# Optimization experiments

Measured on AMD Instinct MI355X. Metric: run time of the kernel, lower is better.

Reference implementation:

```python
import itertools
import jax, jax.numpy as jnp
import numpy as np

# ---- constant tables / bases ----
Y_TABLE_NP = np.array([
    [16, 11, 10, 16, 24, 40, 51, 61],
    [12, 12, 14, 19, 26, 58, 60, 55],
    [14, 13, 16, 24, 40, 57, 69, 56],
    [14, 17, 22, 29, 51, 87, 80, 62],
    [18, 22, 37, 56, 68, 109, 103, 77],
    [24, 35, 55, 64, 81, 104, 113, 92],
    [49, 64, 78, 87, 103, 121, 120, 101],
    [72, 92, 95, 98, 112, 100, 103, 99]], dtype=np.float32)
C_TABLE_NP = np.full((8, 8), 99, dtype=np.float32)
C_TABLE_NP[:4, :4] = np.array([[17, 18, 24, 47], [18, 21, 26, 66],
                               [24, 26, 56, 99], [47, 66, 99, 99]], dtype=np.float32)

def _bases():
    dct = np.zeros((8, 8, 8, 8), dtype=np.float32)
    idct = np.zeros((8, 8, 8, 8), dtype=np.float32)
    for x, y, u, v in itertools.product(range(8), repeat=4):
        dct[x, y, u, v] = np.cos((2 * x + 1) * u * np.pi / 16) * np.cos((2 * y + 1) * v * np.pi / 16)
        idct[x, y, u, v] = np.cos((2 * u + 1) * x * np.pi / 16) * np.cos((2 * v + 1) * y * np.pi / 16)
    alpha = np.array([1.0 / np.sqrt(2)] + [1.0] * 7, dtype=np.float32)
    ao = np.outer(alpha, alpha).astype(np.float32)
    return jnp.asarray(dct), jnp.asarray(ao * 0.25), jnp.asarray(idct), jnp.asarray(ao)

DCT_T, DCT_SCALE, IDCT_T, ALPHA = _bases()
FACTOR = 0.4  # quality_to_factor(80) = (200 - 2*80)/100


def diff_round(x):
    r = jnp.round(x)
    return r + (x - r) ** 3


def _blocks(img):  # (B,H,W) -> (B, H*W/64, 8, 8)
    B, H, W = img.shape
    return img.reshape(B, H // 8, 8, W // 8, 8).transpose(0, 1, 3, 2, 4).reshape(B, -1, 8, 8)


def _merge(patches, H, W):  # (B, N, 8, 8) -> (B, H, W)
    B = patches.shape[0]
    return patches.reshape(B, H // 8, W // 8, 8, 8).transpose(0, 1, 3, 2, 4).reshape(B, H, W)


def setup_inputs() -> dict:
    key = jax.random.key(0)
    image = jax.random.uniform(key, (32, 3, 512, 512), dtype=jnp.float32)
    return {"image": image,
            "y_table": jnp.asarray(Y_TABLE_NP),
            "c_table": jnp.asarray(C_TABLE_NP)}


def reference(image, y_table, c_table):
    B, _, H, W = image.shape
    x = image * 255.0
    # RGB -> YCbCr (matrix stored transposed in torch, tensordot over channel)
    rgb2ycc = jnp.array([[0.299, 0.587, 0.114],
                         [-0.168736, -0.331264, 0.5],
                         [0.5, -0.418688, -0.081312]], dtype=jnp.float32)
    shift = jnp.array([0.0, 128.0, 128.0], dtype=jnp.float32)
    ycc = jnp.einsum('bchw,kc->bhwk', x, rgb2ycc) + shift  # (B,H,W,3)
    y = ycc[..., 0]
    # chroma subsampling: 2x2 average pool
    def pool2(ch):
        return ch.reshape(B, H // 2, 2, W // 2, 2).mean(axis=(2, 4))
    cb = pool2(ycc[..., 1])
    cr = pool2(ycc[..., 2])

    def compress(ch, table):
        blk = _blocks(ch) - 128.0
        d = DCT_SCALE * jnp.einsum('bnxy,xyuv->bnuv', blk, DCT_T)
        return diff_round(d / (table * FACTOR))

    yq = compress(y, y_table)
    cbq = compress(cb, c_table)
    crq = compress(cr, c_table)

    def decompress(q, table, h, w):
        d = (q * (table * FACTOR)) * ALPHA
        blk = 0.25 * jnp.einsum('bnuv,uvxy->bnxy', d, IDCT_T) + 128.0
        return _merge(blk, h, w)

    y_rec = decompress(yq, y_table, H, W)
    cb_rec = decompress(cbq, c_table, H // 2, W // 2)
    cr_rec = decompress(crq, c_table, H // 2, W // 2)

    def up2(ch):
        b, h, w = ch.shape
        return jnp.broadcast_to(ch[:, :, None, :, None], (b, h, 2, w, 2)).reshape(b, 2 * h, 2 * w)

    ycc_rec = jnp.stack([y_rec, up2(cb_rec), up2(cr_rec)], axis=-1)  # (B,H,W,3)
    ycc2rgb = jnp.array([[1.0, 0.0, 1.402],
                         [1.0, -0.344136, -0.714136],
                         [1.0, 1.772, 0.0]], dtype=jnp.float32)
    shift2 = jnp.array([0.0, -128.0, -128.0], dtype=jnp.float32)
    rgb = jnp.einsum('bhwk,ck->bhwc', ycc_rec + shift2, ycc2rgb)
    rgb = rgb.transpose(0, 3, 1, 2)  # (B,3,H,W)
    return jnp.clip(rgb, 0.0, 255.0) / 255.0
```

## Files before the change

kernel.cpp:

```cpp
#include <hip/hip_runtime.h>
#include <math.h>

#define IMG_H 512
#define IMG_W 512
#define IMG_HW (IMG_H * IMG_W)

namespace {

constexpr float CFv[9] = {
    1.0f,
    0.98078528040323044913f,
    0.92387953251128675613f,
    0.83146961230254523708f,
    0.70710678118654752440f,
    0.55557023301960222474f,
    0.38268343236508977173f,
    0.19509032201612826785f,
    0.0f
};

struct CTab {
    float  cf[8][8];
    double cd[8][8];
    float  aof[8][8];
    float  scalef[8][8];
};

constexpr CTab make_ctab() {
    CTab t{};
    for (int y = 0; y < 8; y++) {
        for (int v = 0; v < 8; v++) {
            int a = ((2 * y + 1) * v) & 31;
            if (a > 16) a = 32 - a;
            float val = (a <= 8) ? CFv[a] : -CFv[16 - a];
            t.cf[y][v] = val;
            t.cd[y][v] = (double)val;
        }
    }
    constexpr float A0 = 0.70710678118654752440f;
    for (int u = 0; u < 8; u++) {
        for (int v = 0; v < 8; v++) {
            float au = (u == 0) ? A0 : 1.0f;
            float av = (v == 0) ? A0 : 1.0f;
            float ao = au * av;
            t.aof[u][v] = ao;
            t.scalef[u][v] = ao * 0.25f;
        }
    }
    return t;
}

constexpr CTab CT = make_ctab();

__device__ __forceinline__ void fwd8_d(const double a[8], double s[8]) {
    double e0 = a[0] + a[7], e1 = a[1] + a[6], e2 = a[2] + a[5], e3 = a[3] + a[4];
    double o0 = a[0] - a[7], o1 = a[1] - a[6], o2 = a[2] - a[5], o3 = a[3] - a[4];
    double ee0 = e0 + e3, ee1 = e1 + e2, eo0 = e0 - e3, eo1 = e1 - e2;
    s[0] = ee0 + ee1;
    s[4] = (ee0 - ee1) * CT.cd[0][4];
    s[2] = eo0 * CT.cd[0][2] + eo1 * CT.cd[1][2];
    s[6] = eo0 * CT.cd[0][6] + eo1 * CT.cd[1][6];
    #pragma unroll
    for (int k = 0; k < 4; k++) {
        const int v = 2 * k + 1;
        s[v] = o0 * CT.cd[0][v] + o1 * CT.cd[1][v] + o2 * CT.cd[2][v] + o3 * CT.cd[3][v];
    }
}

__device__ __forceinline__ void inv8_f(const float d[8], float m[8]) {
    float eea = fmaf(CT.cf[0][4], d[4], d[0]);
    float eeb = fmaf(CT.cf[1][4], d[4], d[0]);
    float u2a = d[2] * CT.cf[0][2] + d[6] * CT.cf[0][6];
    float u2b = d[2] * CT.cf[1][2] + d[6] * CT.cf[1][6];
    float E0 = eea + u2a, E1 = eeb + u2b, E2 = eeb - u2b, E3 = eea - u2a;
    float O0 = d[1] * CT.cf[0][1] + d[3] * CT.cf[0][3] + d[5] * CT.cf[0][5] + d[7] * CT.cf[0][7];
    float O1 = d[1] * CT.cf[1][1] + d[3] * CT.cf[1][3] + d[5] * CT.cf[1][5] + d[7] * CT.cf[1][7];
    float O2 = d[1] * CT.cf[2][1] + d[3] * CT.cf[2][3] + d[5] * CT.cf[2][5] + d[7] * CT.cf[2][7];
    float O3 = d[1] * CT.cf[3][1] + d[3] * CT.cf[3][3] + d[5] * CT.cf[3][5] + d[7] * CT.cf[3][7];
    m[0] = E0 + O0; m[7] = E0 - O0;
    m[1] = E1 + O1; m[6] = E1 - O1;
    m[2] = E2 + O2; m[5] = E2 - O2;
    m[3] = E3 + O3; m[4] = E3 - O3;
}

}

#define OFF_CBP 8448
#define OFF_CRP 10624
#define OFF_QYF 12800
#define OFF_QCF 13440
#define OFF_DSY 14080
#define OFF_DSC 14464
#define OFF_CBR 4352
#define OFF_CRR 5504
#define SMEM_BYTES 14848

__global__ void __launch_bounds__(256, 6) djpeg_kernel(
    const float* __restrict__ img,
    const float* __restrict__ ytab,
    const float* __restrict__ ctab,
    float* __restrict__ out)
{
    __shared__ __align__(16) unsigned char smem[SMEM_BYTES];
    double* lY   = (double*)(smem);
    double* cbP  = (double*)(smem + OFF_CBP);
    double* crP  = (double*)(smem + OFF_CRP);
    double* qYfs = (double*)(smem + OFF_QYF);
    double* qCfs = (double*)(smem + OFF_QCF);
    float*  dsY  = (float*)(smem + OFF_DSY);
    float*  dsC  = (float*)(smem + OFF_DSC);
    float*  yR   = (float*)(smem);
    float*  cbR  = (float*)(smem + OFF_CBR);
    float*  crR  = (float*)(smem + OFF_CRR);

    const int t  = threadIdx.x;
    const int X0 = blockIdx.x * 64;
    const int Y0 = blockIdx.y * 16;
    const int bi = blockIdx.z;

    if (t < 128) {
        const float* tab = (t < 64) ? ytab : ctab;
        double* qf = (t < 64) ? qYfs : qCfs;
        float*  df = (t < 64) ? dsY : dsC;
        int e = t & 63, u = e >> 3, v = e & 7;
        float tfacf = tab[e] * 0.4f;
        double tf = (double)tfacf;
        qf[v * 10 + u] = (double)CT.scalef[u][v] / tf;
        df[v * 12 + u] = (float)(tf * (double)CT.aof[u][v]);
    }

    {
        const int xq = t & 15, yb = t >> 4;
        size_t base = ((size_t)bi * 3) * IMG_HW + (size_t)(Y0 + yb) * IMG_W + X0 + xq * 4;
        const float4 rf = *(const float4*)(img + base);
        const float4 gf = *(const float4*)(img + base + IMG_HW);
        const float4 bf = *(const float4*)(img + base + 2 * IMG_HW);
        const double kYR =  (double)0.299f    * 255.0, kYG =  (double)0.587f    * 255.0, kYB =  (double)0.114f    * 255.0;
        const double kbR = -(double)0.168736f * 255.0, kbG = -(double)0.331264f * 255.0, kbB =  (double)0.5f      * 255.0;
        const double krR =  (double)0.5f      * 255.0, krG = -(double)0.418688f * 255.0, krB = -(double)0.081312f * 255.0;
        const float rr[4] = {rf.x, rf.y, rf.z, rf.w};
        const float gg[4] = {gf.x, gf.y, gf.z, gf.w};
        const float bb[4] = {bf.x, bf.y, bf.z, bf.w};
        double Yv[4], Cbv[4], Crv[4];
        #pragma unroll
        for (int i = 0; i < 4; i++) {
            double R = (double)rr[i], G = (double)gg[i], B = (double)bb[i];
            Yv[i]  = kYR * R + kYG * G + kYB * B;
            Cbv[i] = kbR * R + kbG * G + kbB * B + 128.0;
            Crv[i] = krR * R + krG * G + krB * B + 128.0;
        }
        double2* yw = (double2*)(lY + yb * 66 + xq * 4);
        yw[0] = make_double2(Yv[0], Yv[1]);
        yw[1] = make_double2(Yv[2], Yv[3]);
        double cb0 = Cbv[0] + Cbv[1], cb1 = Cbv[2] + Cbv[3];
        double cr0 = Crv[0] + Crv[1], cr1 = Crv[2] + Crv[3];
        cb0 += __shfl_xor(cb0, 16);
        cb1 += __shfl_xor(cb1, 16);
        cr0 += __shfl_xor(cr0, 16);
        cr1 += __shfl_xor(cr1, 16);
        if ((yb & 1) == 0) {
            int pr = yb >> 1;
            *(double2*)(cbP + pr * 34 + xq * 2) = make_double2(cb0 * 0.25, cb1 * 0.25);
            *(double2*)(crP + pr * 34 + xq * 2) = make_double2(cr0 * 0.25, cr1 * 0.25);
        }
    }
    __syncthreads();

    const bool act = (t < 192);
    const int r = t & 7;
    double* blkd = lY;  const double* qfp = qYfs;  const float* dfp = dsY;
    float*  blkf = yR;
    int sD = 66, sF = 68;
    if (t < 128) {
        int g = t >> 3, by = g >> 3, bx = g & 7;
        blkd = lY + (by * 8) * 66 + bx * 8;
        blkf = yR + (by * 8) * 68 + bx * 8;
    } else if (t < 192) {
        int c = t - 128, isCr = c >> 5, g2 = (c >> 3) & 3;
        blkd = (isCr ? crP : cbP) + g2 * 8;
        blkf = (isCr ? crR : cbR) + g2 * 8;
        qfp = qCfs; dfp = dsC;
        sD = 34; sF = 36;
    }

    float dq[8];
    if (act) {
        const double* sp = blkd + r * sD;
        const double2 a01 = *(const double2*)(sp + 0);
        const double2 a23 = *(const double2*)(sp + 2);
        const double2 a45 = *(const double2*)(sp + 4);
        const double2 a67 = *(const double2*)(sp + 6);
        const double a[8] = {a01.x, a01.y, a23.x, a23.y, a45.x, a45.y, a67.x, a67.y};
        double s1[8];
        fwd8_d(a, s1);
        s1[0] -= 1024.0;

        #pragma unroll
        for (int v = 0; v < 8; v++) blkd[v * sD + r] = s1[v];
        asm volatile("s_waitcnt lgkmcnt(0)" ::: "memory");
        const double* rp = blkd + r * sD;
        const double2 b01 = *(const double2*)(rp + 0);
        const double2 b23 = *(const double2*)(rp + 2);
        const double2 b45 = *(const double2*)(rp + 4);
        const double2 b67 = *(const double2*)(rp + 6);
        const double s2[8] = {b01.x, b01.y, b23.x, b23.y, b45.x, b45.y, b67.x, b67.y};

        double D[8];
        fwd8_d(s2, D);
        const double2 f01 = *(const double2*)(qfp + r * 10 + 0);
        const double2 f23 = *(const double2*)(qfp + r * 10 + 2);
        const double2 f45 = *(const double2*)(qfp + r * 10 + 4);
        const double2 f67 = *(const double2*)(qfp + r * 10 + 6);
        const double fsv[8] = {f01.x, f01.y, f23.x, f23.y, f45.x, f45.y, f67.x, f67.y};
        const float4 dA = *(const float4*)(dfp + r * 12);
        const float4 dB = *(const float4*)(dfp + r * 12 + 4);
        const float dsv[8] = {dA.x, dA.y, dA.z, dA.w, dB.x, dB.y, dB.z, dB.w};
        #pragma unroll
        for (int u = 0; u < 8; u++) {
            double xq = D[u] * fsv[u];
            double rq = rint(xq);
            float ef  = (float)(xq - rq);
            float rqf = (float)rq;
            dq[u] = (rqf + ef * ef * ef) * dsv[u];
        }
    }

    __syncthreads();

    if (act) {
        float mc[8];
        inv8_f(dq, mc);

        #pragma unroll
        for (int p = 0; p < 8; p++) blkf[p * sF + r] = mc[p];
        asm volatile("s_waitcnt lgkmcnt(0)" ::: "memory");
        const float* fp_ = blkf + r * sF;
        const float4 m0 = *(const float4*)(fp_);
        const float4 m1 = *(const float4*)(fp_ + 4);
        const float mrow[8] = {m0.x, m0.y, m0.z, m0.w, m1.x, m1.y, m1.z, m1.w};

        float px[8];
        inv8_f(mrow, px);
        float* fw = blkf + r * sF;
        *(float4*)(fw)     = make_float4(fmaf(0.25f, px[0], 128.0f), fmaf(0.25f, px[1], 128.0f),
                                         fmaf(0.25f, px[2], 128.0f), fmaf(0.25f, px[3], 128.0f));
        *(float4*)(fw + 4) = make_float4(fmaf(0.25f, px[4], 128.0f), fmaf(0.25f, px[5], 128.0f),
                                         fmaf(0.25f, px[6], 128.0f), fmaf(0.25f, px[7], 128.0f));
    }
    __syncthreads();

    {
        const int xq = t & 15, yb = t >> 4;
        const float4 yv  = *(const float4*)(yR + yb * 68 + xq * 4);
        const float2 cbv = *(const float2*)(cbR + (yb >> 1) * 36 + xq * 2);
        const float2 crv = *(const float2*)(crR + (yb >> 1) * 36 + xq * 2);
        const float yy[4]  = {yv.x, yv.y, yv.z, yv.w};
        const float cbs[2] = {cbv.x - 128.0f, cbv.y - 128.0f};
        const float crs[2] = {crv.x - 128.0f, crv.y - 128.0f};
        float R4[4], G4[4], B4[4];
        #pragma unroll
        for (int i = 0; i < 4; i++) {
            float Yv = yy[i], Cb = cbs[i >> 1], Cr = crs[i >> 1];
            float Rr = Yv + 1.402f * Cr;
            float Gg = Yv - 0.344136f * Cb - 0.714136f * Cr;
            float Bb = Yv + 1.772f * Cb;
            R4[i] = fminf(fmaxf(Rr, 0.0f), 255.0f) * (1.0f / 255.0f);
            G4[i] = fminf(fmaxf(Gg, 0.0f), 255.0f) * (1.0f / 255.0f);
            B4[i] = fminf(fmaxf(Bb, 0.0f), 255.0f) * (1.0f / 255.0f);
        }
        size_t base = ((size_t)bi * 3) * IMG_HW + (size_t)(Y0 + yb) * IMG_W + X0 + xq * 4;
        *(float4*)(out + base)              = make_float4(R4[0], R4[1], R4[2], R4[3]);
        *(float4*)(out + base + IMG_HW)     = make_float4(G4[0], G4[1], G4[2], G4[3]);
        *(float4*)(out + base + 2 * IMG_HW) = make_float4(B4[0], B4[1], B4[2], B4[3]);
    }
}

extern "C" void kernel_launch(void* const* d_in, const int* in_sizes, int n_in,
                              void* d_out, int out_size, void* d_ws, size_t ws_size,
                              hipStream_t stream) {
    (void)n_in; (void)out_size; (void)d_ws; (void)ws_size;
    const float* img = (const float*)d_in[0];
    const float* yt  = (const float*)d_in[1];
    const float* ct  = (const float*)d_in[2];
    float* out = (float*)d_out;
    int B = in_sizes[0] / (3 * IMG_HW);
    dim3 grid(IMG_W / 64, IMG_H / 16, B);
    djpeg_kernel<<<grid, dim3(256, 1, 1), 0, stream>>>(img, yt, ct, out);
}
```

Baseline: 181.6 us.

## Partition block into per-wave 16x16 tiles and drop block-wide barriers

Each 64-lane wave now owns its own 16x16 pixel tile in shared memory and handles four Y blocks plus one Cb and one Cr block. This removes two of the three block-wide barriers between phases, replacing them with lgkmcnt waits, and the global image loads are hoisted above the table setup so they overlap it. Launch bounds rise from 6 to 8 blocks per CU and shared memory grows slightly. The cost is that 16 of 64 lanes per wave sit idle during the DCT phases, and global loads now cover 16-float row segments instead of 64.

```diff
diff --git a/kernel.cpp b/kernel.cpp
--- a/kernel.cpp
+++ b/kernel.cpp
@@ -85,38 +85,47 @@
 
 }
 
-#define OFF_CBP 8448
-#define OFF_CRP 10624
-#define OFF_QYF 12800
-#define OFF_QCF 13440
-#define OFF_DSY 14080
-#define OFF_DSC 14464
-#define OFF_CBR 4352
-#define OFF_CRR 5504
-#define SMEM_BYTES 14848
-
-__global__ void __launch_bounds__(256, 6) djpeg_kernel(
+#define WAVE_BYTES 3584
+#define OFF_CBP 2304
+#define OFF_CRP 2944
+#define OFF_CBR 1280
+#define OFF_CRR 1664
+#define OFF_QYF 14336
+#define OFF_QCF 14976
+#define OFF_DSY 15616
+#define OFF_DSC 16000
+#define SMEM_BYTES 16384
+
+__global__ void __launch_bounds__(256, 8) djpeg_kernel(
     const float* __restrict__ img,
     const float* __restrict__ ytab,
     const float* __restrict__ ctab,
     float* __restrict__ out)
 {
     __shared__ __align__(16) unsigned char smem[SMEM_BYTES];
-    double* lY   = (double*)(smem);
-    double* cbP  = (double*)(smem + OFF_CBP);
-    double* crP  = (double*)(smem + OFF_CRP);
+    const int t = threadIdx.x;
+    const int w = t >> 6, l = t & 63;
+    unsigned char* wb = smem + w * WAVE_BYTES;
+    double* lYd = (double*)wb;
+    double* cbP = (double*)(wb + OFF_CBP);
+    double* crP = (double*)(wb + OFF_CRP);
+    float*  yR  = (float*)wb;
+    float*  cbR = (float*)(wb + OFF_CBR);
+    float*  crR = (float*)(wb + OFF_CRR);
     double* qYfs = (double*)(smem + OFF_QYF);
     double* qCfs = (double*)(smem + OFF_QCF);
     float*  dsY  = (float*)(smem + OFF_DSY);
     float*  dsC  = (float*)(smem + OFF_DSC);
-    float*  yR   = (float*)(smem);
-    float*  cbR  = (float*)(smem + OFF_CBR);
-    float*  crR  = (float*)(smem + OFF_CRR);
-
-    const int t  = threadIdx.x;
-    const int X0 = blockIdx.x * 64;
+
+    const int bi = blockIdx.z;
+    const int X0 = blockIdx.x * 64 + w * 16;
     const int Y0 = blockIdx.y * 16;
-    const int bi = blockIdx.z;
+    const int q = l & 3, row = l >> 2;
+
+    const size_t base = ((size_t)bi * 3) * IMG_HW + (size_t)(Y0 + row) * IMG_W + X0 + q * 4;
+    const float4 rf = *(const float4*)(img + base);
+    const float4 gf = *(const float4*)(img + base + IMG_HW);
+    const float4 bf = *(const float4*)(img + base + 2 * IMG_HW);
 
     if (t < 128) {
         const float* tab = (t < 64) ? ytab : ctab;
@@ -128,63 +137,56 @@
         qf[v * 10 + u] = (double)CT.scalef[u][v] / tf;
         df[v * 12 + u] = (float)(tf * (double)CT.aof[u][v]);
     }
+    __syncthreads();
 
     {
-        const int xq = t & 15, yb = t >> 4;
-        size_t base = ((size_t)bi * 3) * IMG_HW + (size_t)(Y0 + yb) * IMG_W + X0 + xq * 4;
-        const float4 rf = *(const float4*)(img + base);
-        const float4 gf = *(const float4*)(img + base + IMG_HW);
-        const float4 bf = *(const float4*)(img + base + 2 * IMG_HW);
         const double kYR =  (double)0.299f    * 255.0, kYG =  (double)0.587f    * 255.0, kYB =  (double)0.114f    * 255.0;
         const double kbR = -(double)0.168736f * 255.0, kbG = -(double)0.331264f * 255.0, kbB =  (double)0.5f      * 255.0;
         const double krR =  (double)0.5f      * 255.0, krG = -(double)0.418688f * 255.0, krB = -(double)0.081312f * 255.0;
         const float rr[4] = {rf.x, rf.y, rf.z, rf.w};
         const float gg[4] = {gf.x, gf.y, gf.z, gf.w};
         const float bb[4] = {bf.x, bf.y, bf.z, bf.w};
-        double Yv[4], Cbv[4], Crv[4];
+        double Yv[4];
+        double cb0 = 0.0, cb1 = 0.0, cr0 = 0.0, cr1 = 0.0;
         #pragma unroll
         for (int i = 0; i < 4; i++) {
             double R = (double)rr[i], G = (double)gg[i], B = (double)bb[i];
-            Yv[i]  = kYR * R + kYG * G + kYB * B;
-            Cbv[i] = kbR * R + kbG * G + kbB * B + 128.0;
-            Crv[i] = krR * R + krG * G + krB * B + 128.0;
-        }
-        double2* yw = (double2*)(lY + yb * 66 + xq * 4);
+            Yv[i] = kYR * R + kYG * G + kYB * B;
+            double Cb = kbR * R + kbG * G + kbB * B + 128.0;
+            double Cr = krR * R + krG * G + krB * B + 128.0;
+            if (i < 2) { cb0 += Cb; cr0 += Cr; } else { cb1 += Cb; cr1 += Cr; }
+        }
+        double2* yw = (double2*)(lYd + row * 18 + q * 4);
         yw[0] = make_double2(Yv[0], Yv[1]);
         yw[1] = make_double2(Yv[2], Yv[3]);
-        double cb0 = Cbv[0] + Cbv[1], cb1 = Cbv[2] + Cbv[3];
-        double cr0 = Crv[0] + Crv[1], cr1 = Crv[2] + Crv[3];
-        cb0 += __shfl_xor(cb0, 16);
-        cb1 += __shfl_xor(cb1, 16);
-        cr0 += __shfl_xor(cr0, 16);
-        cr1 += __shfl_xor(cr1, 16);
-        if ((yb & 1) == 0) {
-            int pr = yb >> 1;
-            *(double2*)(cbP + pr * 34 + xq * 2) = make_double2(cb0 * 0.25, cb1 * 0.25);
-            *(double2*)(crP + pr * 34 + xq * 2) = make_double2(cr0 * 0.25, cr1 * 0.25);
-        }
-    }
-    __syncthreads();
-
-    const bool act = (t < 192);
-    const int r = t & 7;
-    double* blkd = lY;  const double* qfp = qYfs;  const float* dfp = dsY;
-    float*  blkf = yR;
-    int sD = 66, sF = 68;
-    if (t < 128) {
-        int g = t >> 3, by = g >> 3, bx = g & 7;
-        blkd = lY + (by * 8) * 66 + bx * 8;
-        blkf = yR + (by * 8) * 68 + bx * 8;
-    } else if (t < 192) {
-        int c = t - 128, isCr = c >> 5, g2 = (c >> 3) & 3;
-        blkd = (isCr ? crP : cbP) + g2 * 8;
-        blkf = (isCr ? crR : cbR) + g2 * 8;
+        cb0 += __shfl_xor(cb0, 4);
+        cb1 += __shfl_xor(cb1, 4);
+        cr0 += __shfl_xor(cr0, 4);
+        cr1 += __shfl_xor(cr1, 4);
+        if ((row & 1) == 0) {
+            const int pr = row >> 1;
+            *(double2*)(cbP + pr * 10 + q * 2) = make_double2(cb0 * 0.25, cb1 * 0.25);
+            *(double2*)(crP + pr * 10 + q * 2) = make_double2(cr0 * 0.25, cr1 * 0.25);
+        }
+    }
+    asm volatile("s_waitcnt lgkmcnt(0)" ::: "memory");
+
+    const int g = l >> 3, r = l & 7;
+    double* blkd = lYd;  float* blkf = yR;
+    const double* qfp = qYfs;  const float* dfp = dsY;
+    int sD = 18, sF = 20;
+    if (g < 4) {
+        const int by = g >> 1, bx = g & 1;
+        blkd = lYd + by * 144 + bx * 8;
+        blkf = yR  + by * 160 + bx * 8;
+    } else {
+        blkd = (g == 5) ? crP : cbP;
+        blkf = (g == 5) ? crR : cbR;
         qfp = qCfs; dfp = dsC;
-        sD = 34; sF = 36;
-    }
-
-    float dq[8];
-    if (act) {
+        sD = 10; sF = 12;
+    }
+
+    if (g < 6) {
         const double* sp = blkd + r * sD;
         const double2 a01 = *(const double2*)(sp + 0);
         const double2 a23 = *(const double2*)(sp + 2);
@@ -215,6 +217,7 @@
         const float4 dA = *(const float4*)(dfp + r * 12);
         const float4 dB = *(const float4*)(dfp + r * 12 + 4);
         const float dsv[8] = {dA.x, dA.y, dA.z, dA.w, dB.x, dB.y, dB.z, dB.w};
+        float dq[8];
         #pragma unroll
         for (int u = 0; u < 8; u++) {
             double xq = D[u] * fsv[u];
@@ -223,11 +226,7 @@
             float rqf = (float)rq;
             dq[u] = (rqf + ef * ef * ef) * dsv[u];
         }
-    }
-
-    __syncthreads();
-
-    if (act) {
+
         float mc[8];
         inv8_f(dq, mc);
 
@@ -247,13 +246,12 @@
         *(float4*)(fw + 4) = make_float4(fmaf(0.25f, px[4], 128.0f), fmaf(0.25f, px[5], 128.0f),
                                          fmaf(0.25f, px[6], 128.0f), fmaf(0.25f, px[7], 128.0f));
     }
-    __syncthreads();
+    asm volatile("s_waitcnt lgkmcnt(0)" ::: "memory");
 
     {
-        const int xq = t & 15, yb = t >> 4;
-        const float4 yv  = *(const float4*)(yR + yb * 68 + xq * 4);
-        const float2 cbv = *(const float2*)(cbR + (yb >> 1) * 36 + xq * 2);
-        const float2 crv = *(const float2*)(crR + (yb >> 1) * 36 + xq * 2);
+        const float4 yv  = *(const float4*)(yR + row * 20 + q * 4);
+        const float2 cbv = *(const float2*)(cbR + (row >> 1) * 12 + q * 2);
+        const float2 crv = *(const float2*)(crR + (row >> 1) * 12 + q * 2);
         const float yy[4]  = {yv.x, yv.y, yv.z, yv.w};
         const float cbs[2] = {cbv.x - 128.0f, cbv.y - 128.0f};
         const float crs[2] = {crv.x - 128.0f, crv.y - 128.0f};
@@ -268,7 +266,6 @@
             G4[i] = fminf(fmaxf(Gg, 0.0f), 255.0f) * (1.0f / 255.0f);
             B4[i] = fminf(fmaxf(Bb, 0.0f), 255.0f) * (1.0f / 255.0f);
         }
-        size_t base = ((size_t)bi * 3) * IMG_HW + (size_t)(Y0 + yb) * IMG_W + X0 + xq * 4;
         *(float4*)(out + base)              = make_float4(R4[0], R4[1], R4[2], R4[3]);
         *(float4*)(out + base + IMG_HW)     = make_float4(G4[0], G4[1], G4[2], G4[3]);
         *(float4*)(out + base + 2 * IMG_HW) = make_float4(B4[0], B4[1], B4[2], B4[3]);
```

After: 185.7 us. +2.3%, slower.

## Process two 16-row strips per block to amortize setup and overlap loads

Applied to the files above, without the earlier changes.

Each block now handles a 64x32 tile as two 16-row strips with separate shared-memory buffers, halving the grid. All six global float4 loads are issued up front, before the quantization-table setup, so their latency overlaps that setup. The table setup, barriers and launch overhead are amortized over twice the work, and per-thread ILP rises from interleaving two independent DCT pipelines. In exchange shared memory nearly doubles, register pressure rises, and launch bounds drop from 6 to 5 blocks per CU, which may lower occupancy.

```diff
diff --git a/kernel.cpp b/kernel.cpp
--- a/kernel.cpp
+++ b/kernel.cpp
@@ -85,38 +85,55 @@
 
 }
 
+#define STRIP_BYTES 12800
 #define OFF_CBP 8448
 #define OFF_CRP 10624
-#define OFF_QYF 12800
-#define OFF_QCF 13440
-#define OFF_DSY 14080
-#define OFF_DSC 14464
 #define OFF_CBR 4352
 #define OFF_CRR 5504
-#define SMEM_BYTES 14848
-
-__global__ void __launch_bounds__(256, 6) djpeg_kernel(
+#define OFF_QYF 25600
+#define OFF_QCF 26240
+#define OFF_DSY 26880
+#define OFF_DSC 27264
+#define SMEM_BYTES 27648
+
+__global__ void __launch_bounds__(256, 5) djpeg_kernel(
     const float* __restrict__ img,
     const float* __restrict__ ytab,
     const float* __restrict__ ctab,
     float* __restrict__ out)
 {
     __shared__ __align__(16) unsigned char smem[SMEM_BYTES];
-    double* lY   = (double*)(smem);
-    double* cbP  = (double*)(smem + OFF_CBP);
-    double* crP  = (double*)(smem + OFF_CRP);
+    double* lY0  = (double*)(smem);
+    double* cbP0 = (double*)(smem + OFF_CBP);
+    double* crP0 = (double*)(smem + OFF_CRP);
+    float*  yR0  = (float*)(smem);
+    float*  cbR0 = (float*)(smem + OFF_CBR);
+    float*  crR0 = (float*)(smem + OFF_CRR);
+    double* lY1  = (double*)(smem + STRIP_BYTES);
+    double* cbP1 = (double*)(smem + STRIP_BYTES + OFF_CBP);
+    double* crP1 = (double*)(smem + STRIP_BYTES + OFF_CRP);
+    float*  yR1  = (float*)(smem + STRIP_BYTES);
+    float*  cbR1 = (float*)(smem + STRIP_BYTES + OFF_CBR);
+    float*  crR1 = (float*)(smem + STRIP_BYTES + OFF_CRR);
     double* qYfs = (double*)(smem + OFF_QYF);
     double* qCfs = (double*)(smem + OFF_QCF);
     float*  dsY  = (float*)(smem + OFF_DSY);
     float*  dsC  = (float*)(smem + OFF_DSC);
-    float*  yR   = (float*)(smem);
-    float*  cbR  = (float*)(smem + OFF_CBR);
-    float*  crR  = (float*)(smem + OFF_CRR);
 
     const int t  = threadIdx.x;
     const int X0 = blockIdx.x * 64;
-    const int Y0 = blockIdx.y * 16;
+    const int Y0 = blockIdx.y * 32;
     const int bi = blockIdx.z;
+    const int xq = t & 15, yb = t >> 4;
+
+    const size_t base0 = ((size_t)bi * 3) * IMG_HW + (size_t)(Y0 + yb) * IMG_W + X0 + xq * 4;
+    const size_t base1 = base0 + (size_t)16 * IMG_W;
+    const float4 rf0 = *(const float4*)(img + base0);
+    const float4 gf0 = *(const float4*)(img + base0 + IMG_HW);
+    const float4 bf0 = *(const float4*)(img + base0 + 2 * IMG_HW);
+    const float4 rf1 = *(const float4*)(img + base1);
+    const float4 gf1 = *(const float4*)(img + base1 + IMG_HW);
+    const float4 bf1 = *(const float4*)(img + base1 + 2 * IMG_HW);
 
     if (t < 128) {
         const float* tab = (t < 64) ? ytab : ctab;
@@ -129,128 +146,179 @@
         df[v * 12 + u] = (float)(tf * (double)CT.aof[u][v]);
     }
 
-    {
-        const int xq = t & 15, yb = t >> 4;
-        size_t base = ((size_t)bi * 3) * IMG_HW + (size_t)(Y0 + yb) * IMG_W + X0 + xq * 4;
-        const float4 rf = *(const float4*)(img + base);
-        const float4 gf = *(const float4*)(img + base + IMG_HW);
-        const float4 bf = *(const float4*)(img + base + 2 * IMG_HW);
+    auto phase1 = [&](const float4 rf, const float4 gf, const float4 bf,
+                      double* lY, double* cbP, double* crP) {
         const double kYR =  (double)0.299f    * 255.0, kYG =  (double)0.587f    * 255.0, kYB =  (double)0.114f    * 255.0;
         const double kbR = -(double)0.168736f * 255.0, kbG = -(double)0.331264f * 255.0, kbB =  (double)0.5f      * 255.0;
         const double krR =  (double)0.5f      * 255.0, krG = -(double)0.418688f * 255.0, krB = -(double)0.081312f * 255.0;
         const float rr[4] = {rf.x, rf.y, rf.z, rf.w};
         const float gg[4] = {gf.x, gf.y, gf.z, gf.w};
         const float bb[4] = {bf.x, bf.y, bf.z, bf.w};
-        double Yv[4], Cbv[4], Crv[4];
+        double Yv[4];
+        double cb0 = 0.0, cb1 = 0.0, cr0 = 0.0, cr1 = 0.0;
         #pragma unroll
         for (int i = 0; i < 4; i++) {
             double R = (double)rr[i], G = (double)gg[i], B = (double)bb[i];
-            Yv[i]  = kYR * R + kYG * G + kYB * B;
-            Cbv[i] = kbR * R + kbG * G + kbB * B + 128.0;
-            Crv[i] = krR * R + krG * G + krB * B + 128.0;
+            Yv[i] = kYR * R + kYG * G + kYB * B;
+            double Cb = kbR * R + kbG * G + kbB * B + 128.0;
+            double Cr = krR * R + krG * G + krB * B + 128.0;
+            if (i < 2) { cb0 += Cb; cr0 += Cr; } else { cb1 += Cb; cr1 += Cr; }
         }
         double2* yw = (double2*)(lY + yb * 66 + xq * 4);
         yw[0] = make_double2(Yv[0], Yv[1]);
         yw[1] = make_double2(Yv[2], Yv[3]);
-        double cb0 = Cbv[0] + Cbv[1], cb1 = Cbv[2] + Cbv[3];
-        double cr0 = Crv[0] + Crv[1], cr1 = Crv[2] + Crv[3];
         cb0 += __shfl_xor(cb0, 16);
         cb1 += __shfl_xor(cb1, 16);
         cr0 += __shfl_xor(cr0, 16);
         cr1 += __shfl_xor(cr1, 16);
         if ((yb & 1) == 0) {
-            int pr = yb >> 1;
+            const int pr = yb >> 1;
             *(double2*)(cbP + pr * 34 + xq * 2) = make_double2(cb0 * 0.25, cb1 * 0.25);
             *(double2*)(crP + pr * 34 + xq * 2) = make_double2(cr0 * 0.25, cr1 * 0.25);
         }
-    }
+    };
+    phase1(rf0, gf0, bf0, lY0, cbP0, crP0);
+    phase1(rf1, gf1, bf1, lY1, cbP1, crP1);
     __syncthreads();
 
     const bool act = (t < 192);
     const int r = t & 7;
-    double* blkd = lY;  const double* qfp = qYfs;  const float* dfp = dsY;
-    float*  blkf = yR;
-    int sD = 66, sF = 68;
+    int eD = 0, eF = 0, sD = 66, sF = 68;
+    const double* qfp = qYfs;  const float* dfp = dsY;
     if (t < 128) {
         int g = t >> 3, by = g >> 3, bx = g & 7;
-        blkd = lY + (by * 8) * 66 + bx * 8;
-        blkf = yR + (by * 8) * 68 + bx * 8;
-    } else if (t < 192) {
+        eD = (by * 8) * 66 + bx * 8;
+        eF = (by * 8) * 68 + bx * 8;
+    } else {
         int c = t - 128, isCr = c >> 5, g2 = (c >> 3) & 3;
-        blkd = (isCr ? crP : cbP) + g2 * 8;
-        blkf = (isCr ? crR : cbR) + g2 * 8;
+        eD = (isCr ? (OFF_CRP / 8) : (OFF_CBP / 8)) + g2 * 8;
+        eF = (isCr ? (OFF_CRR / 4) : (OFF_CBR / 4)) + g2 * 8;
         qfp = qCfs; dfp = dsC;
         sD = 34; sF = 36;
     }
-
-    float dq[8];
+    double* bdA = lY0 + eD;  double* bdB = lY1 + eD;
+    float*  bfA = yR0 + eF;  float*  bfB = yR1 + eF;
+
+    float dqA[8], dqB[8];
     if (act) {
-        const double* sp = blkd + r * sD;
-        const double2 a01 = *(const double2*)(sp + 0);
-        const double2 a23 = *(const double2*)(sp + 2);
-        const double2 a45 = *(const double2*)(sp + 4);
-        const double2 a67 = *(const double2*)(sp + 6);
-        const double a[8] = {a01.x, a01.y, a23.x, a23.y, a45.x, a45.y, a67.x, a67.y};
-        double s1[8];
-        fwd8_d(a, s1);
-        s1[0] -= 1024.0;
-
-        #pragma unroll
-        for (int v = 0; v < 8; v++) blkd[v * sD + r] = s1[v];
+        {
+            const double* sp = bdA + r * sD;
+            const double2 a01 = *(const double2*)(sp + 0);
+            const double2 a23 = *(const double2*)(sp + 2);
+            const double2 a45 = *(const double2*)(sp + 4);
+            const double2 a67 = *(const double2*)(sp + 6);
+            const double a[8] = {a01.x, a01.y, a23.x, a23.y, a45.x, a45.y, a67.x, a67.y};
+            double s1[8];
+            fwd8_d(a, s1);
+            s1[0] -= 1024.0;
+            #pragma unroll
+            for (int v = 0; v < 8; v++) bdA[v * sD + r] = s1[v];
+        }
+        {
+            const double* sp = bdB + r * sD;
+            const double2 a01 = *(const double2*)(sp + 0);
+            const double2 a23 = *(const double2*)(sp + 2);
+            const double2 a45 = *(const double2*)(sp + 4);
+            const double2 a67 = *(const double2*)(sp + 6);
+            const double a[8] = {a01.x, a01.y, a23.x, a23.y, a45.x, a45.y, a67.x, a67.y};
+            double s1[8];
+            fwd8_d(a, s1);
+            s1[0] -= 1024.0;
+            #pragma unroll
+            for (int v = 0; v < 8; v++) bdB[v * sD + r] = s1[v];
+        }
         asm volatile("s_waitcnt lgkmcnt(0)" ::: "memory");
-        const double* rp = blkd + r * sD;
-        const double2 b01 = *(const double2*)(rp + 0);
-        const double2 b23 = *(const double2*)(rp + 2);
-        const double2 b45 = *(const double2*)(rp + 4);
-        const double2 b67 = *(const double2*)(rp + 6);
-        const double s2[8] = {b01.x, b01.y, b23.x, b23.y, b45.x, b45.y, b67.x, b67.y};
-
-        double D[8];
-        fwd8_d(s2, D);
+
         const double2 f01 = *(const double2*)(qfp + r * 10 + 0);
         const double2 f23 = *(const double2*)(qfp + r * 10 + 2);
         const double2 f45 = *(const double2*)(qfp + r * 10 + 4);
         const double2 f67 = *(const double2*)(qfp + r * 10 + 6);
         const double fsv[8] = {f01.x, f01.y, f23.x, f23.y, f45.x, f45.y, f67.x, f67.y};
-        const float4 dA = *(const float4*)(dfp + r * 12);
-        const float4 dB = *(const float4*)(dfp + r * 12 + 4);
-        const float dsv[8] = {dA.x, dA.y, dA.z, dA.w, dB.x, dB.y, dB.z, dB.w};
+        const float4 dA4 = *(const float4*)(dfp + r * 12);
+        const float4 dB4 = *(const float4*)(dfp + r * 12 + 4);
+        const float dsv[8] = {dA4.x, dA4.y, dA4.z, dA4.w, dB4.x, dB4.y, dB4.z, dB4.w};
+
+        {
+            const double* rp = bdA + r * sD;
+            const double2 b01 = *(const double2*)(rp + 0);
+            const double2 b23 = *(const double2*)(rp + 2);
+            const double2 b45 = *(const double2*)(rp + 4);
+            const double2 b67 = *(const double2*)(rp + 6);
+            const double s2[8] = {b01.x, b01.y, b23.x, b23.y, b45.x, b45.y, b67.x, b67.y};
+            double D[8];
+            fwd8_d(s2, D);
+            #pragma unroll
+            for (int u = 0; u < 8; u++) {
+                double xqv = D[u] * fsv[u];
+                double rq = rint(xqv);
+                float ef  = (float)(xqv - rq);
+                float rqf = (float)rq;
+                dqA[u] = (rqf + ef * ef * ef) * dsv[u];
+            }
+        }
+        {
+            const double* rp = bdB + r * sD;
+            const double2 b01 = *(const double2*)(rp + 0);
+            const double2 b23 = *(const double2*)(rp + 2);
+            const double2 b45 = *(const double2*)(rp + 4);
+            const double2 b67 = *(const double2*)(rp + 6);
+            const double s2[8] = {b01.x, b01.y, b23.x, b23.y, b45.x, b45.y, b67.x, b67.y};
+            double D[8];
+            fwd8_d(s2, D);
+            #pragma unroll
+            for (int u = 0; u < 8; u++) {
+                double xqv = D[u] * fsv[u];
+                double rq = rint(xqv);
+                float ef  = (float)(xqv - rq);
+                float rqf = (float)rq;
+                dqB[u] = (rqf + ef * ef * ef) * dsv[u];
+            }
+        }
+    }
+
+    __syncthreads();
+
+    if (act) {
+        float mcA[8], mcB[8];
+        inv8_f(dqA, mcA);
+        inv8_f(dqB, mcB);
         #pragma unroll
-        for (int u = 0; u < 8; u++) {
-            double xq = D[u] * fsv[u];
-            double rq = rint(xq);
-            float ef  = (float)(xq - rq);
-            float rqf = (float)rq;
-            dq[u] = (rqf + ef * ef * ef) * dsv[u];
-        }
-    }
-
+        for (int p = 0; p < 8; p++) bfA[p * sF + r] = mcA[p];
+        #pragma unroll
+        for (int p = 0; p < 8; p++) bfB[p * sF + r] = mcB[p];
+        asm volatile("s_waitcnt lgkmcnt(0)" ::: "memory");
+
+        {
+            const float* fp_ = bfA + r * sF;
+            const float4 m0 = *(const float4*)(fp_);
+            const float4 m1 = *(const float4*)(fp_ + 4);
+            const float mrow[8] = {m0.x, m0.y, m0.z, m0.w, m1.x, m1.y, m1.z, m1.w};
+            float px[8];
+            inv8_f(mrow, px);
+            float* fw = bfA + r * sF;
+            *(float4*)(fw)     = make_float4(fmaf(0.25f, px[0], 128.0f), fmaf(0.25f, px[1], 128.0f),
+                                             fmaf(0.25f, px[2], 128.0f), fmaf(0.25f, px[3], 128.0f));
+            *(float4*)(fw + 4) = make_float4(fmaf(0.25f, px[4], 128.0f), fmaf(0.25f, px[5], 128.0f),
+                                             fmaf(0.25f, px[6], 128.0f), fmaf(0.25f, px[7], 128.0f));
+        }
+        {
+            const float* fp_ = bfB + r * sF;
+            const float4 m0 = *(const float4*)(fp_);
+            const float4 m1 = *(const float4*)(fp_ + 4);
+            const float mrow[8] = {m0.x, m0.y, m0.z, m0.w, m1.x, m1.y, m1.z, m1.w};
+            float px[8];
+            inv8_f(mrow, px);
+            float* fw = bfB + r * sF;
+            *(float4*)(fw)     = make_float4(fmaf(0.25f, px[0], 128.0f), fmaf(0.25f, px[1], 128.0f),
+                                             fmaf(0.25f, px[2], 128.0f), fmaf(0.25f, px[3], 128.0f));
+            *(float4*)(fw + 4) = make_float4(fmaf(0.25f, px[4], 128.0f), fmaf(0.25f, px[5], 128.0f),
+                                             fmaf(0.25f, px[6], 128.0f), fmaf(0.25f, px[7], 128.0f));
+        }
+    }
     __syncthreads();
 
-    if (act) {
-        float mc[8];
-        inv8_f(dq, mc);
-
-        #pragma unroll
-        for (int p = 0; p < 8; p++) blkf[p * sF + r] = mc[p];
-        asm volatile("s_waitcnt lgkmcnt(0)" ::: "memory");
-        const float* fp_ = blkf + r * sF;
-        const float4 m0 = *(const float4*)(fp_);
-        const float4 m1 = *(const float4*)(fp_ + 4);
-        const float mrow[8] = {m0.x, m0.y, m0.z, m0.w, m1.x, m1.y, m1.z, m1.w};
-
-        float px[8];
-        inv8_f(mrow, px);
-        float* fw = blkf + r * sF;
-        *(float4*)(fw)     = make_float4(fmaf(0.25f, px[0], 128.0f), fmaf(0.25f, px[1], 128.0f),
-                                         fmaf(0.25f, px[2], 128.0f), fmaf(0.25f, px[3], 128.0f));
-        *(float4*)(fw + 4) = make_float4(fmaf(0.25f, px[4], 128.0f), fmaf(0.25f, px[5], 128.0f),
-                                         fmaf(0.25f, px[6], 128.0f), fmaf(0.25f, px[7], 128.0f));
-    }
-    __syncthreads();
-
-    {
-        const int xq = t & 15, yb = t >> 4;
+    auto phase3 = [&](const float* yR, const float* cbR, const float* crR,
+                      const size_t base) {
         const float4 yv  = *(const float4*)(yR + yb * 68 + xq * 4);
         const float2 cbv = *(const float2*)(cbR + (yb >> 1) * 36 + xq * 2);
         const float2 crv = *(const float2*)(crR + (yb >> 1) * 36 + xq * 2);
@@ -268,11 +336,12 @@
             G4[i] = fminf(fmaxf(Gg, 0.0f), 255.0f) * (1.0f / 255.0f);
             B4[i] = fminf(fmaxf(Bb, 0.0f), 255.0f) * (1.0f / 255.0f);
         }
-        size_t base = ((size_t)bi * 3) * IMG_HW + (size_t)(Y0 + yb) * IMG_W + X0 + xq * 4;
         *(float4*)(out + base)              = make_float4(R4[0], R4[1], R4[2], R4[3]);
         *(float4*)(out + base + IMG_HW)     = make_float4(G4[0], G4[1], G4[2], G4[3]);
         *(float4*)(out + base + 2 * IMG_HW) = make_float4(B4[0], B4[1], B4[2], B4[3]);
-    }
+    };
+    phase3(yR0, cbR0, crR0, base0);
+    phase3(yR1, cbR1, crR1, base1);
 }
 
 extern "C" void kernel_launch(void* const* d_in, const int* in_sizes, int n_in,
@@ -284,6 +353,6 @@
     const float* ct  = (const float*)d_in[2];
     float* out = (float*)d_out;
     int B = in_sizes[0] / (3 * IMG_HW);
-    dim3 grid(IMG_W / 64, IMG_H / 16, B);
+    dim3 grid(IMG_W / 64, IMG_H / 32, B);
     djpeg_kernel<<<grid, dim3(256, 1, 1), 0, stream>>>(img, yt, ct, out);
 }
```

Result: no change. 181.7 us (+0.1%).
